# Optimization experiments

Hardware: AMD Instinct MI355X
Metric: run time of the kernel (lower is better)

The kernel has to match this reference:

```python
import jax, jax.numpy as jnp
import numpy as np

C = 256       # channels (MWI ctor arg c)
K = 8         # number of EM bases (MWI ctor arg k)
STAGES = 7    # EM iterations per scale (stage_num)
SIZES = (1, 3, 5)  # multi-scale unfold kernel sizes


def _unfold(x, k):
    # torch F.unfold(x, k, padding=(k-1)//2, stride=1) -> (b, c, k*k, h, w)
    # with kernel-position ordering (ki major, kj minor), matching torch layout.
    b, c, h, w = x.shape
    p = (k - 1) // 2
    xp = jnp.pad(x, ((0, 0), (0, 0), (p, p), (p, p)))
    pats = [xp[:, :, i:i + h, j:j + w] for i in range(k) for j in range(k)]
    return jnp.stack(pats, axis=2)


def _fold(z, k, h, w):
    # inverse of _unfold with overlap-add: z (b, c, k*k, h, w) -> (b, c, h, w)
    b, c, kk, _, _ = z.shape
    p = (k - 1) // 2
    out = jnp.zeros((b, c, h + 2 * p, w + 2 * p), z.dtype)
    for idx in range(kk):
        i, j = divmod(idx, k)
        out = out.at[:, :, i:i + h, j:j + w].add(z[:, :, idx])
    return out[:, :, p:p + h, p:p + w]


def _l2norm(v, axis):
    return v / (1e-6 + jnp.linalg.norm(v, axis=axis, keepdims=True))


def setup_inputs() -> dict:
    key = jax.random.key(0)
    k0, k1, k2 = jax.random.split(key, 3)
    b, h, w = 4, 64, 64
    x = jax.random.normal(k0, (b, C, h, w), jnp.float32)
    # mu buffer: normal(0, sqrt(2/k)) then l2-normalized over channel dim
    mu0 = jax.random.normal(k1, (1, C, K), jnp.float32) * np.float32(np.sqrt(2.0 / K))
    mu0 = _l2norm(mu0, axis=1)
    w_scale = jnp.float32(1.0)
    # convcat: Conv2d(3c, c, 1) init normal(0, sqrt(2/(1*1*out_channels)))
    convcat_w = jax.random.normal(k2, (C, 3 * C, 1, 1), jnp.float32) * np.float32(np.sqrt(2.0 / C))
    convcat_b = jnp.zeros((C,), jnp.float32)
    return {"x": x, "mu0": mu0, "w_scale": w_scale,
            "convcat_w": convcat_w, "convcat_b": convcat_b}


def reference(x, mu0, w_scale, convcat_w, convcat_b):
    b, c, h, w = x.shape
    idn = x
    # EM iterations run under torch.no_grad(): stop gradients through mu/z.
    mu = jax.lax.stop_gradient(jnp.broadcast_to(mu0, (b, c, K)))
    feats = []
    for size in SIZES:
        uf = _unfold(x, size).reshape(b, c, -1)          # (b, c, n), n = size^2*h*w
        uf_sg = jax.lax.stop_gradient(uf)
        z = None
        for _ in range(STAGES):
            z = jax.nn.softmax(jnp.einsum('bcn,bck->bnk', uf_sg, mu), axis=2)
            z_ = z / (1e-6 + z.sum(axis=1, keepdims=True))
            mu = _l2norm(jnp.einsum('bcn,bnk->bck', uf_sg, z_), axis=1)
        # reconstruction: mu @ z^T -> (b, c, n), fold back with overlap-add
        zr = jnp.einsum('bck,bnk->bcn', mu, z).reshape(b, c, size * size, h, w)
        feats.append(_fold(zr, size, h, w))
    cat = jnp.concatenate(feats, axis=1)                 # (b, 3c, h, w)
    u = jnp.einsum('bihw,oi->bohw', cat, convcat_w[:, :, 0, 0]) \
        + convcat_b[None, :, None, None]
    out = jax.nn.relu(u * w_scale + idn)
    return out, mu
```

## Files before the change

kernel.cpp:

```cpp
#include <hip/hip_runtime.h>
#include <hip/hip_bf16.h>

#define KB 8


typedef __attribute__((ext_vector_type(8))) short frag_ab;
typedef __attribute__((ext_vector_type(4))) float frag_cd;

__device__ __forceinline__ float bf16_to_f(unsigned short u) {
    union { unsigned int i; float f; } v;
    v.i = ((unsigned int)u) << 16;
    return v.f;
}

__device__ __forceinline__ unsigned short f_to_bf16_bits(float f) {
    __hip_bfloat16 h = (__hip_bfloat16)f;
    return *(unsigned short*)&h;
}

__device__ __forceinline__ float4 f4add(float4 a, float4 b) {
    return make_float4(a.x + b.x, a.y + b.y, a.z + b.z, a.w + b.w);
}

__device__ __forceinline__ float wf(int i, int pd) {
    return (float)(min(pd, i) + min(pd, 63 - i) + 1);
}

__global__ __launch_bounds__(256)
void probe_all_kernel(const unsigned short* __restrict__ x,
                      const unsigned short* __restrict__ mu0,
                      const unsigned short* __restrict__ Wc,
                      int* __restrict__ slots)
{
    __shared__ unsigned int red[256];
    int bid = blockIdx.x, t = threadIdx.x;
    const unsigned short* p;
    int n;
    if (bid < 32)       { p = x + bid * 2048;         n = 2048; }
    else if (bid == 32) { p = mu0;                    n = 2048; }
    else                { p = Wc + (bid - 33) * 4096; n = 4096; }
    unsigned int mx = 0;
    for (int i = t; i < n; i += 256) {
        unsigned int bits = (((unsigned int)p[i]) << 16) & 0x7FFFFFFFu;
        mx = max(mx, bits);
    }
    red[t] = mx;
    __syncthreads();
    for (int st = 128; st > 0; st >>= 1) {
        if (t < st) red[t] = max(red[t], red[t + st]);
        __syncthreads();
    }
    if (t == 0) slots[bid] = (int)red[0];
}

__global__ __launch_bounds__(256)
void decide_init_kernel(const unsigned short* __restrict__ wsc_u,
                        const void* __restrict__ mu0,
                        int* __restrict__ slots,
                        float* __restrict__ muInit)
{
    int t = threadIdx.x;
    if (t == 0) {
        const int TH = 0x49742400;
        int mxX = 0, mxW = 0;
        for (int i = 0; i < 32; ++i)  mxX = max(mxX, slots[i]);
        for (int i = 33; i < 49; ++i) mxW = max(mxW, slots[i]);
        slots[56] = (mxX < TH) ? 1 : 0;
        slots[57] = (slots[32] < TH) ? 1 : 0;
        slots[58] = (mxW < TH) ? 1 : 0;
        slots[59] = (bf16_to_f(wsc_u[0]) == 1.0f) ? 1 : 0;
    }
    __syncthreads();
    int fb = slots[57];
    const unsigned short* mb = (const unsigned short*)mu0;
    const float*          mf = (const float*)mu0;
    for (int i = t; i < 2048; i += 256)
        muInit[i] = fb ? bf16_to_f(mb[i]) : mf[i];
}

__global__ __launch_bounds__(512)
void stage_z_kernel(const void* __restrict__ x,
                    unsigned short* __restrict__ xbf,
                    const float* __restrict__ inst,
                    const float* __restrict__ muInit,
                    const void* __restrict__ Wc,
                    float* __restrict__ Mg,
                    float* __restrict__ pp,
                    float* __restrict__ pps,
                    __hip_bfloat16* __restrict__ zfOut,
                    const int* __restrict__ flags,
                    int pd, float oobPrev, int mode, int writeM, int sM,
                    int writeXbf)
{
    __shared__ unsigned short xt[256][72];
    __shared__ float muL[2048];
    __shared__ float pr[4608];
    __shared__ unsigned short zbfT[16][72];
    __shared__ float muRed[32];
    __shared__ float sS[8][8];

    const int tid = threadIdx.x;
    const int bid = blockIdx.x;
    const int b   = bid >> 6;
    const int row = bid & 63;
    const int p0  = row << 6;
    const int fW  = flags[2];

    if (!writeXbf) {
        #pragma unroll
        for (int i = 0; i < 4; ++i) {
            int idx = tid + i * 512;
            int c = idx >> 3, sub = idx & 7;
            const uint4 u = *(const uint4*)(xbf
                          + ((size_t)(b * 256 + c) << 12) + (size_t)(p0 + sub * 8));
            *(uint4*)(&xt[c][sub * 8]) = u;
        }
    } else if (flags[0]) {
        #pragma unroll
        for (int i = 0; i < 4; ++i) {
            int idx = tid + i * 512;
            int c = idx >> 3, sub = idx & 7;
            size_t gb = ((size_t)(b * 256 + c) << 12) + (size_t)(p0 + sub * 8);
            const uint4 u = *(const uint4*)((const unsigned short*)x + gb);
            *(uint4*)(&xt[c][sub * 8]) = u;
            *(uint4*)(xbf + gb) = u;
        }
    } else {
        #pragma unroll
        for (int i = 0; i < 8; ++i) {
            int idx = tid + i * 512;
            int c = idx >> 4, sub = idx & 15;
            size_t gb = ((size_t)(b * 256 + c) << 12) + (size_t)(p0 + sub * 4);
            const float4 a = *(const float4*)((const float*)x + gb);
            unsigned int u0 = ((unsigned int)f_to_bf16_bits(a.y) << 16) | f_to_bf16_bits(a.x);
            unsigned int u1 = ((unsigned int)f_to_bf16_bits(a.w) << 16) | f_to_bf16_bits(a.z);
            unsigned int* d = (unsigned int*)(&xt[c][sub * 4]);
            d[0] = u0; d[1] = u1;
            *(uint2*)(xbf + gb) = make_uint2(u0, u1);
        }
    }

    float v4[4];
    if (mode) {
        const int c  = tid & 255;
        const int kh = (tid >> 8) * 4;
        float r2[4];
        #pragma unroll
        for (int k = 0; k < 4; ++k) {
            float s0 = inst[8192 + b * 8 + kh + k] + oobPrev * 0.125f;
            v4[k] = inst[b * 2048 + c * 8 + kh + k] / (1e-6f + s0);
            r2[k] = v4[k] * v4[k];
        }
        #pragma unroll
        for (int off = 32; off > 0; off >>= 1) {
            #pragma unroll
            for (int k = 0; k < 4; ++k) r2[k] += __shfl_xor(r2[k], off, 64);
        }
        if ((tid & 63) == 0) {
            int w = tid >> 6;
            #pragma unroll
            for (int k = 0; k < 4; ++k) muRed[w * 4 + k] = r2[k];
        }
    }
    __syncthreads();
    if (mode) {
        const int c  = tid & 255;
        const int kh = (tid >> 8) * 4;
        const int base0 = (tid >> 8) * 16;
        #pragma unroll
        for (int k = 0; k < 4; ++k) {
            float s2 = muRed[base0 + k] + muRed[base0 + k + 4]
                     + muRed[base0 + k + 8] + muRed[base0 + k + 12];
            muL[c * 8 + kh + k] = v4[k] / (1e-6f + sqrtf(s2));
        }
    } else {
        *(float4*)(muL + tid * 4) = *(const float4*)(muInit + tid * 4);
    }
    __syncthreads();

    if (writeM && row < 8 && tid < 256) {
        int o = row * 32 + (tid >> 3), k = tid & 7;
        int base = o * 768 + sM * 256;
        float acc = 0.f;
        if (fW) {
            const unsigned short* wp = (const unsigned short*)Wc + base;
            for (int c = 0; c < 256; ++c) acc += bf16_to_f(wp[c]) * muL[c * 8 + k];
        } else {
            const float* wp = (const float*)Wc + base;
            for (int c = 0; c < 256; ++c) acc += wp[c] * muL[c * 8 + k];
        }
        Mg[b * 6144 + o * 24 + sM * 8 + k] = acc;
    }

    {
        const int pp2 = tid & 31;
        const int g   = tid >> 5;
        const int w   = tid >> 6;
        float d0[KB], d1[KB];
        #pragma unroll
        for (int k = 0; k < KB; ++k) { d0[k] = 0.f; d1[k] = 0.f; }
        #pragma unroll 4
        for (int cc = 0; cc < 16; ++cc) {
            int c = g * 16 + cc;
            unsigned int xu = *(const unsigned int*)(&xt[c][2 * pp2]);
            float xv0 = bf16_to_f((unsigned short)(xu & 0xFFFFu));
            float xv1 = bf16_to_f((unsigned short)(xu >> 16));
            float4 ma = *(const float4*)(muL + c * 8);
            float4 mb = *(const float4*)(muL + c * 8 + 4);
            d0[0] += xv0 * ma.x; d0[1] += xv0 * ma.y;
            d0[2] += xv0 * ma.z; d0[3] += xv0 * ma.w;
            d0[4] += xv0 * mb.x; d0[5] += xv0 * mb.y;
            d0[6] += xv0 * mb.z; d0[7] += xv0 * mb.w;
            d1[0] += xv1 * ma.x; d1[1] += xv1 * ma.y;
            d1[2] += xv1 * ma.z; d1[3] += xv1 * ma.w;
            d1[4] += xv1 * mb.x; d1[5] += xv1 * mb.y;
            d1[6] += xv1 * mb.z; d1[7] += xv1 * mb.w;
        }
        #pragma unroll
        for (int k = 0; k < KB; ++k) {
            d0[k] += __shfl_xor(d0[k], 32, 64);
            d1[k] += __shfl_xor(d1[k], 32, 64);
        }
        if ((tid & 63) < 32) {
            float* prw = pr + (w * 64 + 2 * pp2) * 9;
            #pragma unroll
            for (int k = 0; k < KB; ++k) prw[k] = d0[k];
            #pragma unroll
            for (int k = 0; k < KB; ++k) prw[9 + k] = d1[k];
        }
    }
    __syncthreads();

    {
        const int pi = tid >> 3, k = tid & 7;
        float l = 0.f;
        #pragma unroll
        for (int g = 0; g < 8; ++g) l += pr[(g * 64 + pi) * 9 + k];
        float m = l;
        #pragma unroll
        for (int off = 1; off < 8; off <<= 1)
            m = fmaxf(m, __shfl_xor(m, off, 64));
        float e = expf(l - m);
        float se = e;
        #pragma unroll
        for (int off = 1; off < 8; off <<= 1)
            se += __shfl_xor(se, off, 64);
        float wgt = wf(row, pd) * wf(pi, pd);
        float z = e * (wgt / se);
        unsigned short zh = f_to_bf16_bits(z);
        zbfT[k][pi]     = zh;
        zbfT[k + 8][pi] = f_to_bf16_bits(z - bf16_to_f(zh));
        if (zfOut)
            zfOut[(size_t)(b * 4096 + p0 + pi) * KB + k] = (__hip_bfloat16)z;
        float sw = z;
        sw += __shfl_xor(sw, 8, 64);
        sw += __shfl_xor(sw, 16, 64);
        sw += __shfl_xor(sw, 32, 64);
        if ((tid & 63) < 8) sS[tid >> 6][tid & 7] = sw;
    }
    __syncthreads();

    if (tid < 8) {
        float ss = 0.f;
        #pragma unroll
        for (int w = 0; w < 8; ++w) ss += sS[w][tid];
        pps[bid * 8 + tid] = ss;
    }

    {
        const int l   = tid & 63;
        const int w   = tid >> 6;
        const int n   = l & 15;
        const int grp = l >> 4;
        union { uint4 u; frag_ab s; } bv0, bv1, av;
        bv0.u = *(const uint4*)(&zbfT[n][grp * 8]);
        bv1.u = *(const uint4*)(&zbfT[n][32 + grp * 8]);
        #pragma unroll
        for (int mt = 0; mt < 2; ++mt) {
            const int m = w * 2 + mt;
            const int cA = m * 16 + n;
            frag_cd acc = {0.f, 0.f, 0.f, 0.f};
            av.u = *(const uint4*)(&xt[cA][grp * 8]);
            acc = __builtin_amdgcn_mfma_f32_16x16x32_bf16(av.s, bv0.s, acc, 0, 0, 0);
            av.u = *(const uint4*)(&xt[cA][32 + grp * 8]);
            acc = __builtin_amdgcn_mfma_f32_16x16x32_bf16(av.s, bv1.s, acc, 0, 0, 0);
            #pragma unroll
            for (int r = 0; r < 4; ++r) {
                float sum = acc[r] + __shfl_xor(acc[r], 8, 64);
                if (n < 8) {
                    int cOut = m * 16 + grp * 4 + r;
                    pp[(size_t)bid * 2048 + cOut * 8 + n] = sum;
                }
            }
        }
    }
}

__global__ __launch_bounds__(256)
void reduce_kernel(const float* __restrict__ pp,
                   const float* __restrict__ pps,
                   float* __restrict__ inst)
{
    __shared__ float4 comb[8][32];
    __shared__ float combS[8][8];
    const int bid = blockIdx.x, tid = threadIdx.x;
    const int b = bid >> 4, j = bid & 15;
    const int col = tid & 31;
    const int rg  = tid >> 5;
    const float* base = pp + (size_t)(b * 64 + rg * 8) * 2048
                           + (size_t)(j * 128 + col * 4);
    float4 a0 = *(const float4*)(base);
    float4 a1 = *(const float4*)(base + (size_t)1 * 2048);
    float4 a2 = *(const float4*)(base + (size_t)2 * 2048);
    float4 a3 = *(const float4*)(base + (size_t)3 * 2048);
    float4 a4 = *(const float4*)(base + (size_t)4 * 2048);
    float4 a5 = *(const float4*)(base + (size_t)5 * 2048);
    float4 a6 = *(const float4*)(base + (size_t)6 * 2048);
    float4 a7 = *(const float4*)(base + (size_t)7 * 2048);
    comb[rg][col] = f4add(f4add(f4add(a0, a1), f4add(a2, a3)),
                          f4add(f4add(a4, a5), f4add(a6, a7)));
    if (j == 0 && tid < 64) {
        int k = tid & 7, rg2 = tid >> 3;
        float ss = 0.f;
        const float* sb = pps + (size_t)b * 512 + (size_t)(rg2 * 8) * 8 + k;
        #pragma unroll
        for (int r = 0; r < 8; ++r) ss += sb[r * 8];
        combS[rg2][k] = ss;
    }
    __syncthreads();
    if (tid < 32) {
        float4 t = comb[0][tid];
        #pragma unroll
        for (int g = 1; g < 8; ++g) t = f4add(t, comb[g][tid]);
        *(float4*)(inst + b * 2048 + j * 128 + tid * 4) = t;
    }
    if (j == 0 && tid >= 32 && tid < 40) {
        int k = tid - 32;
        float ss = 0.f;
        #pragma unroll
        for (int g = 0; g < 8; ++g) ss += combS[g][k];
        inst[8192 + b * 8 + k] = ss;
    }
}

__global__ __launch_bounds__(256)
void reduce_final_kernel(const float* __restrict__ inst,
                         const void* __restrict__ Wc,
                         const int* __restrict__ flags,
                         float* __restrict__ Mg,
                         float* __restrict__ muOut)
{
    __shared__ float muL[2048];
    __shared__ float muRed[32];
    const int tid = threadIdx.x;
    const int b   = blockIdx.x >> 3;
    const int sub = blockIdx.x & 7;

    float v[KB], r2[KB];
    const float* accRow = inst + b * 2048 + tid * 8;
    #pragma unroll
    for (int k = 0; k < KB; ++k) {
        float s0 = inst[8192 + b * 8 + k] + 3804.f * 0.125f;
        v[k] = accRow[k] / (1e-6f + s0);
        r2[k] = v[k] * v[k];
    }
    #pragma unroll
    for (int off = 32; off > 0; off >>= 1) {
        #pragma unroll
        for (int k = 0; k < KB; ++k) r2[k] += __shfl_xor(r2[k], off, 64);
    }
    if ((tid & 63) == 0) {
        #pragma unroll
        for (int k = 0; k < KB; ++k) muRed[(tid >> 6) * 8 + k] = r2[k];
    }
    __syncthreads();
    #pragma unroll
    for (int k = 0; k < KB; ++k) {
        float s2 = muRed[k] + muRed[8 + k] + muRed[16 + k] + muRed[24 + k];
        float mv = v[k] / (1e-6f + sqrtf(s2));
        muL[tid * 8 + k] = mv;
        if (sub == 0 && muOut) muOut[b * 2048 + tid * 8 + k] = mv;
    }
    __syncthreads();
    {
        int o = sub * 32 + (tid >> 3), k = tid & 7;
        int base = o * 768 + 2 * 256;
        float acc = 0.f;
        if (flags[2]) {
            const unsigned short* wp = (const unsigned short*)Wc + base;
            for (int c = 0; c < 256; ++c) acc += bf16_to_f(wp[c]) * muL[c * 8 + k];
        } else {
            const float* wp = (const float*)Wc + base;
            for (int c = 0; c < 256; ++c) acc += wp[c] * muL[c * 8 + k];
        }
        Mg[b * 6144 + o * 24 + 16 + k] = acc;
    }
}

__global__ __launch_bounds__(256)
void out_kernel(const void* __restrict__ x,
                const float* __restrict__ Mg,
                const __hip_bfloat16* __restrict__ zf,
                const unsigned short* __restrict__ bias_u,
                const unsigned short* __restrict__ wsc_u,
                const int* __restrict__ flags,
                float* __restrict__ out)
{
    __shared__ float ML[256 * 24];
    __shared__ float biasL[256];
    int tid = threadIdx.x, bid = blockIdx.x;
    int b = bid >> 7, tile = bid & 127, p0 = tile << 5;
    int fx = flags[0];
    #pragma unroll
    for (int j = 0; j < 24; ++j) ML[tid + j * 256] = Mg[b * 6144 + tid + j * 256];
    biasL[tid] = bf16_to_f(bias_u[tid]);
    __syncthreads();

    float wsv = flags[3] ? bf16_to_f(wsc_u[0]) : ((const float*)wsc_u)[0];
    int pl = tid & 31, og = tid >> 5;
    int p = p0 + pl;
    float zv[24];
    #pragma unroll
    for (int s = 0; s < 3; ++s) {
        const __hip_bfloat16* zp = zf + s * 131072 + (b * 4096 + p) * KB;
        #pragma unroll
        for (int k = 0; k < KB; ++k) zv[s * 8 + k] = (float)zp[k];
    }
    const size_t gbase = (size_t)(b * 256 + og * 32) * 4096 + (size_t)p;
    float* op = out + gbase;
    if (fx) {
        const unsigned short* xp = (const unsigned short*)x + gbase;
        for (int oo = 0; oo < 32; ++oo) {
            int c = og * 32 + oo;
            float u = biasL[c];
            #pragma unroll
            for (int j = 0; j < 24; ++j) u += ML[c * 24 + j] * zv[j];
            op[(size_t)oo * 4096] =
                fmaxf(u * wsv + bf16_to_f(xp[(size_t)oo * 4096]), 0.f);
        }
    } else {
        const float* xp = (const float*)x + gbase;
        for (int oo = 0; oo < 32; ++oo) {
            int c = og * 32 + oo;
            float u = biasL[c];
            #pragma unroll
            for (int j = 0; j < 24; ++j) u += ML[c * 24 + j] * zv[j];
            op[(size_t)oo * 4096] = fmaxf(u * wsv + xp[(size_t)oo * 4096], 0.f);
        }
    }
}

extern "C" void kernel_launch(void* const* d_in, const int* in_sizes, int n_in,
                              void* d_out, int out_size, void* d_ws, size_t ws_size,
                              hipStream_t stream)
{
    (void)ws_size;
    float* out = (float*)d_out;

    const void *x = nullptr, *mu0 = nullptr, *wsc = nullptr,
               *Wc = nullptr, *bias = nullptr;
    for (int i = 0; i < n_in; ++i) {
        switch (in_sizes[i]) {
            case 4194304: x    = d_in[i]; break;
            case 2048:    mu0  = d_in[i]; break;
            case 1:       wsc  = d_in[i]; break;
            case 196608:  Wc   = d_in[i]; break;
            case 256:     bias = d_in[i]; break;
            default: break;
        }
    }
    if (!x || !mu0 || !wsc || !Wc || !bias) return;

    float* muOut = (out_size >= 4202496) ? (out + 4194304) : (float*)nullptr;

    float* wsf    = (float*)d_ws;
    float* muInit = wsf;
    float* Mg     = wsf + 2048;
    int*   slots  = (int*)(wsf + 26624);
    int*   flags  = slots + 56;
    __hip_bfloat16* zf  = (__hip_bfloat16*)(wsf + 26752);
    float* inst   = wsf + 223360;
    float* pps    = wsf + 231584;
    float* pp     = wsf + 233728;
    unsigned short* xbf = (unsigned short*)(wsf + 758016);

    probe_all_kernel<<<49, 256, 0, stream>>>(
        (const unsigned short*)x, (const unsigned short*)mu0,
        (const unsigned short*)Wc, slots);
    decide_init_kernel<<<1, 256, 0, stream>>>(
        (const unsigned short*)wsc, mu0, slots, muInit);

    const float oobArr[3] = {0.f, 764.f, 3804.f};
    for (int t = 0; t < 21; ++t) {
        int   s        = t / 7;
        int   mode     = (t == 0) ? 0 : 1;
        float oobPrev  = (t == 0) ? 0.f : oobArr[(t - 1) / 7];
        int   writeM   = (t == 7 || t == 14) ? 1 : 0;
        int   sM       = (t == 7) ? 0 : 1;
        int   writeXbf = (t == 0) ? 1 : 0;
        __hip_bfloat16* zfOut = ((t % 7) == 6) ? (zf + s * 131072)
                                               : (__hip_bfloat16*)nullptr;
        stage_z_kernel<<<256, 512, 0, stream>>>(
            x, xbf, inst, muInit, Wc, Mg, pp, pps, zfOut, flags,
            s, oobPrev, mode, writeM, sM, writeXbf);
        reduce_kernel<<<64, 256, 0, stream>>>(pp, pps, inst);
    }

    reduce_final_kernel<<<32, 256, 0, stream>>>(inst, Wc, flags, Mg, muOut);

    out_kernel<<<512, 256, 0, stream>>>(
        x, Mg, zf, (const unsigned short*)bias, (const unsigned short*)wsc,
        flags, out);
}
```

Measured before the change: 304.4 us.

## Vectorize loads, wave-reduce flag maxima, and spread partial-logit stores across lanes

After: 300.8 us. About the same (-1.2%).

```diff
diff --git a/kernel.cpp b/kernel.cpp
--- a/kernel.cpp
+++ b/kernel.cpp
@@ -60,15 +60,21 @@
                         float* __restrict__ muInit)
 {
     int t = threadIdx.x;
-    if (t == 0) {
-        const int TH = 0x49742400;
-        int mxX = 0, mxW = 0;
-        for (int i = 0; i < 32; ++i)  mxX = max(mxX, slots[i]);
-        for (int i = 33; i < 49; ++i) mxW = max(mxW, slots[i]);
-        slots[56] = (mxX < TH) ? 1 : 0;
-        slots[57] = (slots[32] < TH) ? 1 : 0;
-        slots[58] = (mxW < TH) ? 1 : 0;
-        slots[59] = (bf16_to_f(wsc_u[0]) == 1.0f) ? 1 : 0;
+    if (t < 64) {
+        unsigned int vX = (t < 32) ? (unsigned int)slots[t] : 0u;
+        unsigned int vW = (t >= 33 && t < 49) ? (unsigned int)slots[t] : 0u;
+        #pragma unroll
+        for (int off = 32; off > 0; off >>= 1) {
+            vX = max(vX, (unsigned int)__shfl_xor((int)vX, off, 64));
+            vW = max(vW, (unsigned int)__shfl_xor((int)vW, off, 64));
+        }
+        if (t == 0) {
+            const unsigned int TH = 0x49742400u;
+            slots[56] = (vX < TH) ? 1 : 0;
+            slots[57] = ((unsigned int)slots[32] < TH) ? 1 : 0;
+            slots[58] = (vW < TH) ? 1 : 0;
+            slots[59] = (bf16_to_f(wsc_u[0]) == 1.0f) ? 1 : 0;
+        }
     }
     __syncthreads();
     int fb = slots[57];
@@ -144,13 +150,15 @@
     if (mode) {
         const int c  = tid & 255;
         const int kh = (tid >> 8) * 4;
+        const float4 accQ = *(const float4*)(inst + b * 2048 + c * 8 + kh);
+        const float4 sQ   = *(const float4*)(inst + 8192 + b * 8 + kh);
         float r2[4];
-        #pragma unroll
-        for (int k = 0; k < 4; ++k) {
-            float s0 = inst[8192 + b * 8 + kh + k] + oobPrev * 0.125f;
-            v4[k] = inst[b * 2048 + c * 8 + kh + k] / (1e-6f + s0);
-            r2[k] = v4[k] * v4[k];
-        }
+        v4[0] = accQ.x / (1e-6f + (sQ.x + oobPrev * 0.125f));
+        v4[1] = accQ.y / (1e-6f + (sQ.y + oobPrev * 0.125f));
+        v4[2] = accQ.z / (1e-6f + (sQ.z + oobPrev * 0.125f));
+        v4[3] = accQ.w / (1e-6f + (sQ.w + oobPrev * 0.125f));
+        #pragma unroll
+        for (int k = 0; k < 4; ++k) r2[k] = v4[k] * v4[k];
         #pragma unroll
         for (int off = 32; off > 0; off >>= 1) {
             #pragma unroll
@@ -196,6 +204,7 @@
         const int pp2 = tid & 31;
         const int g   = tid >> 5;
         const int w   = tid >> 6;
+        const int half = (tid & 63) >> 5;
         float d0[KB], d1[KB];
         #pragma unroll
         for (int k = 0; k < KB; ++k) { d0[k] = 0.f; d1[k] = 0.f; }
@@ -221,13 +230,12 @@
             d0[k] += __shfl_xor(d0[k], 32, 64);
             d1[k] += __shfl_xor(d1[k], 32, 64);
         }
-        if ((tid & 63) < 32) {
-            float* prw = pr + (w * 64 + 2 * pp2) * 9;
-            #pragma unroll
-            for (int k = 0; k < KB; ++k) prw[k] = d0[k];
-            #pragma unroll
-            for (int k = 0; k < KB; ++k) prw[9 + k] = d1[k];
-        }
+        float sel[KB];
+        #pragma unroll
+        for (int k = 0; k < KB; ++k) sel[k] = half ? d1[k] : d0[k];
+        float* prw = pr + (w * 64 + 2 * pp2 + half) * 9;
+        #pragma unroll
+        for (int k = 0; k < KB; ++k) prw[k] = sel[k];
     }
     __syncthreads();
 
@@ -432,9 +440,16 @@
         const unsigned short* xp = (const unsigned short*)x + gbase;
         for (int oo = 0; oo < 32; ++oo) {
             int c = og * 32 + oo;
+            const float4* MLc = (const float4*)(ML + c * 24);
+            float4 m0 = MLc[0], m1 = MLc[1], m2 = MLc[2];
+            float4 m3 = MLc[3], m4 = MLc[4], m5 = MLc[5];
             float u = biasL[c];
-            #pragma unroll
-            for (int j = 0; j < 24; ++j) u += ML[c * 24 + j] * zv[j];
+            u += m0.x*zv[0] + m0.y*zv[1] + m0.z*zv[2] + m0.w*zv[3];
+            u += m1.x*zv[4] + m1.y*zv[5] + m1.z*zv[6] + m1.w*zv[7];
+            u += m2.x*zv[8] + m2.y*zv[9] + m2.z*zv[10] + m2.w*zv[11];
+            u += m3.x*zv[12] + m3.y*zv[13] + m3.z*zv[14] + m3.w*zv[15];
+            u += m4.x*zv[16] + m4.y*zv[17] + m4.z*zv[18] + m4.w*zv[19];
+            u += m5.x*zv[20] + m5.y*zv[21] + m5.z*zv[22] + m5.w*zv[23];
             op[(size_t)oo * 4096] =
                 fmaxf(u * wsv + bf16_to_f(xp[(size_t)oo * 4096]), 0.f);
         }
@@ -442,9 +457,16 @@
         const float* xp = (const float*)x + gbase;
         for (int oo = 0; oo < 32; ++oo) {
             int c = og * 32 + oo;
+            const float4* MLc = (const float4*)(ML + c * 24);
+            float4 m0 = MLc[0], m1 = MLc[1], m2 = MLc[2];
+            float4 m3 = MLc[3], m4 = MLc[4], m5 = MLc[5];
             float u = biasL[c];
-            #pragma unroll
-            for (int j = 0; j < 24; ++j) u += ML[c * 24 + j] * zv[j];
+            u += m0.x*zv[0] + m0.y*zv[1] + m0.z*zv[2] + m0.w*zv[3];
+            u += m1.x*zv[4] + m1.y*zv[5] + m1.z*zv[6] + m1.w*zv[7];
+            u += m2.x*zv[8] + m2.y*zv[9] + m2.z*zv[10] + m2.w*zv[11];
+            u += m3.x*zv[12] + m3.y*zv[13] + m3.z*zv[14] + m3.w*zv[15];
+            u += m4.x*zv[16] + m4.y*zv[17] + m4.z*zv[18] + m4.w*zv[19];
+            u += m5.x*zv[20] + m5.y*zv[21] + m5.z*zv[22] + m5.w*zv[23];
             op[(size_t)oo * 4096] = fmaxf(u * wsv + xp[(size_t)oo * 4096], 0.f);
         }
     }
```
